# Performance work log

Measured on AMD Instinct MI355X. Metric: run time of the kernel, lower is better.

Reference implementation:

```python
import jax, jax.numpy as jnp
import numpy as np

DIM = 2048
N_HEADS = 16
HEAD_DIM = DIM // N_HEADS
WINDOW = 256
B, S = 2, 2048


def setup_inputs() -> dict:
    key = jax.random.key(0)
    kx, kq, kk, kv, ko = jax.random.split(key, 5)
    bound = 1.0 / np.sqrt(DIM)  # nn.Linear default init range
    x = jax.random.normal(kx, (B, S, DIM), dtype=jnp.float32)
    wq = jax.random.uniform(kq, (DIM, DIM), jnp.float32, -bound, bound)
    wk = jax.random.uniform(kk, (DIM, DIM), jnp.float32, -bound, bound)
    wv = jax.random.uniform(kv, (DIM, DIM), jnp.float32, -bound, bound)
    wo = jax.random.uniform(ko, (DIM, DIM), jnp.float32, -bound, bound)
    return {"x": x, "wq": wq, "wk": wk, "wv": wv, "wo": wo}


def reference(x, wq, wk, wv, wo):
    b, s, d = x.shape
    scale = HEAD_DIM ** -0.5
    # projections (torch Linear: y = x @ W.T)
    q = (x @ wq.T).reshape(b, s, N_HEADS, HEAD_DIM)
    k = (x @ wk.T).reshape(b, s, N_HEADS, HEAD_DIM)
    v = (x @ wv.T).reshape(b, s, N_HEADS, HEAD_DIM)
    # scores: [b, h, i, j]
    scores = jnp.einsum("bihd,bjhd->bhij", q, k) * scale
    # faithful mask: (all-ones, window cleared, then triu(1)) == mask iff j - i > window//2
    idx = jnp.arange(s)
    mask = (idx[None, :] - idx[:, None]) > (WINDOW // 2)  # [s, s] bool, True = masked
    scores = jnp.where(mask[None, None, :, :], -jnp.inf, scores)
    attn = jax.nn.softmax(scores, axis=-1)
    out = jnp.einsum("bhij,bjhd->bihd", attn, v).reshape(b, s, d)
    return out @ wo.T
```

## Files before the change

### kernel.cpp

```cpp
#include <hip/hip_runtime.h>
#include <stdint.h>
#include <stddef.h>

#define DIMN 2048
#define NH 16
#define HD 128
#define SEQ 2048
#define WIN 128

typedef __attribute__((ext_vector_type(4))) float f32x4;
typedef __attribute__((ext_vector_type(8))) short bf16x8;
typedef __attribute__((ext_vector_type(4))) int i32x4;

#define AS1 __attribute__((address_space(1)))
#define AS3 __attribute__((address_space(3)))

__device__ __forceinline__ unsigned short f2bf(float f) {
  union { float f; unsigned u; } v; v.f = f;
  unsigned r = v.u + 0x7FFFu + ((v.u >> 16) & 1u);
  return (unsigned short)(r >> 16);
}

__global__ void cast_bf16_kernel(const float* __restrict__ src,
                                 unsigned short* __restrict__ dst, int n4) {
  int i = blockIdx.x * blockDim.x + threadIdx.x;
  const int stride = gridDim.x * blockDim.x;
  for (; i < n4; i += stride) {
    float4 v = ((const float4*)src)[i];
    ushort4 o;
    o.x = f2bf(v.x); o.y = f2bf(v.y); o.z = f2bf(v.z); o.w = f2bf(v.w);
    ((ushort4*)dst)[i] = o;
  }
}

__global__ void cast4_bf16_kernel(const float* __restrict__ s0, const float* __restrict__ s1,
                                  const float* __restrict__ s2, const float* __restrict__ s3,
                                  unsigned short* __restrict__ dst, int n4) {
  const float* s = (blockIdx.y == 0) ? s0 : (blockIdx.y == 1) ? s1 : (blockIdx.y == 2) ? s2 : s3;
  unsigned short* d = dst + (size_t)blockIdx.y * 4194304;
  int i = blockIdx.x * blockDim.x + threadIdx.x;
  const int stride = gridDim.x * blockDim.x;
  for (; i < n4; i += stride) {
    float4 v = ((const float4*)s)[i];
    ushort4 o;
    o.x = f2bf(v.x); o.y = f2bf(v.y); o.z = f2bf(v.z); o.w = f2bf(v.w);
    ((ushort4*)d)[i] = o;
  }
}

__device__ __forceinline__ void gemm_mainloop_g128(
    const unsigned short* __restrict__ A, const unsigned short* __restrict__ B,
    int m0, int n0, unsigned short* As, unsigned short* Bs, f32x4 acc[4][4]) {
  const int t = threadIdx.x, lane = t & 63, wid = t >> 6;
  const int c = lane & 15, g = lane >> 4;
  const int wr = wid >> 1, wc = wid & 1;

  const int srow = wid * 32 + (lane >> 3);
  const int gslot = (lane & 7) ^ (lane >> 3);
  const unsigned short* ga = A + (size_t)(m0 + srow) * DIMN + gslot * 8;
  const unsigned short* gb = B + (size_t)(n0 + srow) * DIMN + gslot * 8;
  unsigned short* la = As + (size_t)(wid * 32) * 64;
  unsigned short* lb = Bs + (size_t)(wid * 32) * 64;

  const int swc = c & 7;

  for (int k0 = 0; k0 < DIMN; k0 += 64) {
    __syncthreads();
#pragma unroll
    for (int i = 0; i < 4; ++i) {
      __builtin_amdgcn_global_load_lds(
          (const AS1 unsigned*)(ga + (size_t)i * 8 * DIMN + k0),
          (AS3 unsigned*)(la + i * 8 * 64), 16, 0, 0);
      __builtin_amdgcn_global_load_lds(
          (const AS1 unsigned*)(gb + (size_t)i * 8 * DIMN + k0),
          (AS3 unsigned*)(lb + i * 8 * 64), 16, 0, 0);
    }
    __syncthreads();
#pragma unroll
    for (int kk = 0; kk < 2; ++kk) {
      bf16x8 af[4], bfv[4];
#pragma unroll
      for (int mi = 0; mi < 4; ++mi)
        af[mi] = *(const bf16x8*)&As[(wr * 64 + mi * 16 + c) * 64 +
                                     (((kk * 4 + g) ^ swc) * 8)];
#pragma unroll
      for (int ni = 0; ni < 4; ++ni)
        bfv[ni] = *(const bf16x8*)&Bs[(wc * 64 + ni * 16 + c) * 64 +
                                      (((kk * 4 + g) ^ swc) * 8)];
#pragma unroll
      for (int mi = 0; mi < 4; ++mi)
#pragma unroll
        for (int ni = 0; ni < 4; ++ni)
          acc[mi][ni] = __builtin_amdgcn_mfma_f32_16x16x32_bf16(
              af[mi], bfv[ni], acc[mi][ni], 0, 0, 0);
    }
  }
}

__global__ __launch_bounds__(256, 3) void gemm_qkv_kernel(
    const unsigned short* __restrict__ Xb,
    const unsigned short* __restrict__ Wq,
    const unsigned short* __restrict__ Wk,
    const unsigned short* __restrict__ Wv,
    unsigned short* __restrict__ Qb,
    unsigned short* __restrict__ Kb,
    unsigned short* __restrict__ Vt) {
  __shared__ __attribute__((aligned(16))) unsigned short As[128 * 64];
  __shared__ __attribute__((aligned(16))) unsigned short Bs[128 * 64];
  const int z = blockIdx.z;
  const unsigned short* W = (z == 0) ? Wq : (z == 1) ? Wk : Wv;
  const int m0 = blockIdx.y * 128, n0 = blockIdx.x * 128;

  f32x4 acc[4][4];
  const f32x4 zv = {0.f, 0.f, 0.f, 0.f};
#pragma unroll
  for (int i = 0; i < 4; ++i)
#pragma unroll
    for (int j = 0; j < 4; ++j) acc[i][j] = zv;

  gemm_mainloop_g128(Xb, W, m0, n0, As, Bs, acc);

  const int lane = threadIdx.x & 63, wid = threadIdx.x >> 6;
  const int c = lane & 15, g = lane >> 4;
  const int wr = wid >> 1, wc = wid & 1;
  unsigned short* Out01 = (z == 0) ? Qb : Kb;
#pragma unroll
  for (int mi = 0; mi < 4; ++mi) {
#pragma unroll
    for (int ni = 0; ni < 4; ++ni) {
      const int mrow = m0 + wr * 64 + mi * 16 + g * 4;
      const int ncol = n0 + wc * 64 + ni * 16 + c;
      const int h = ncol >> 7, d = ncol & 127;
      const int b = mrow >> 11, s = mrow & 2047;
      if (z < 2) {
#pragma unroll
        for (int j = 0; j < 4; ++j)
          Out01[((size_t)(b * NH + h) * SEQ + s + j) * HD + d] =
              f2bf(acc[mi][ni][j]);
      } else {
        ushort4 pk;
        pk.x = f2bf(acc[mi][ni][0]); pk.y = f2bf(acc[mi][ni][1]);
        pk.z = f2bf(acc[mi][ni][2]); pk.w = f2bf(acc[mi][ni][3]);
        *(ushort4*)&Vt[((size_t)(b * NH + h) * HD + d) * SEQ + s] = pk;
      }
    }
  }
}

__global__ __launch_bounds__(256, 3) void gemm_out_kernel(
    const unsigned short* __restrict__ Ab,
    const unsigned short* __restrict__ Wo,
    float* __restrict__ Cf) {
  __shared__ __attribute__((aligned(16))) unsigned short As[128 * 64];
  __shared__ __attribute__((aligned(16))) unsigned short Bs[128 * 64];
  const int m0 = blockIdx.y * 128, n0 = blockIdx.x * 128;

  f32x4 acc[4][4];
  const f32x4 zv = {0.f, 0.f, 0.f, 0.f};
#pragma unroll
  for (int i = 0; i < 4; ++i)
#pragma unroll
    for (int j = 0; j < 4; ++j) acc[i][j] = zv;

  gemm_mainloop_g128(Ab, Wo, m0, n0, As, Bs, acc);

  const int lane = threadIdx.x & 63, wid = threadIdx.x >> 6;
  const int c = lane & 15, g = lane >> 4;
  const int wr = wid >> 1, wc = wid & 1;
#pragma unroll
  for (int mi = 0; mi < 4; ++mi) {
#pragma unroll
    for (int ni = 0; ni < 4; ++ni) {
      const int mrow = m0 + wr * 64 + mi * 16 + g * 4;
      const int ncol = n0 + wc * 64 + ni * 16 + c;
#pragma unroll
      for (int j = 0; j < 4; ++j)
        Cf[(size_t)(mrow + j) * DIMN + ncol] = acc[mi][ni][j];
    }
  }
}

__global__ __launch_bounds__(256, 2) void attn_kernel(
    const unsigned short* __restrict__ Qg,
    const unsigned short* __restrict__ Kg,
    const unsigned short* __restrict__ Vtg,
    unsigned short* __restrict__ Og) {
  __shared__ __attribute__((aligned(16))) unsigned short Ks[64 * 128];
  __shared__ __attribute__((aligned(16))) unsigned short Vs[128 * 64];
  __shared__ __attribute__((aligned(16))) unsigned short Ps[4 * 32 * 64];

  const int bh = blockIdx.x;
  const int yy = blockIdx.y;
  const int qt = (yy < 8) ? yy : 23 - yy;
  const int q0 = qt * 128;
  const int t = threadIdx.x, wid = t >> 6, lane = t & 63;
  const int c = lane & 15, g = lane >> 4;
  const int swc = c & 7;

  const unsigned short* Kbh = Kg + (size_t)bh * SEQ * HD;
  const unsigned short* Vbh = Vtg + (size_t)bh * HD * SEQ;

  bf16x8 qf[2][4];
#pragma unroll
  for (int mi = 0; mi < 2; ++mi) {
    const unsigned short* qb =
        Qg + ((size_t)bh * SEQ + q0 + wid * 32 + mi * 16 + c) * HD + g * 8;
#pragma unroll
    for (int kk = 0; kk < 4; ++kk) qf[mi][kk] = *(const bf16x8*)(qb + kk * 32);
  }

  f32x4 o[2][8];
  const f32x4 zv = {0.f, 0.f, 0.f, 0.f};
#pragma unroll
  for (int mi = 0; mi < 2; ++mi)
#pragma unroll
    for (int ni = 0; ni < 8; ++ni) o[mi][ni] = zv;
  float M[2][4], L[2][4];
#pragma unroll
  for (int mi = 0; mi < 2; ++mi)
#pragma unroll
    for (int j = 0; j < 4; ++j) { M[mi][j] = -1e30f; L[mi][j] = 0.f; }

  const int ntA = (q0 + 256) >> 6;
  const int nt = (ntA < (SEQ >> 6)) ? ntA : (SEQ >> 6);
  const float kl2e = 0.08838834764831845f * 1.4426950408889634f;

  const int kswz = (t & 15) ^ ((t >> 4) & 7);
  const int vswz = (t & 7) ^ ((t >> 3) & 7);
  const int kgo = (t >> 4) * HD + (t & 15) * 8;
  const int klo = (t >> 4) * 128 + kswz * 8;
  const int vlo = (t >> 3) * 64 + vswz * 8;
  const size_t vgo = (size_t)(t >> 3) * SEQ + (t & 7) * 8;

  i32x4 kc[4], vc[4];
#pragma unroll
  for (int r = 0; r < 4; ++r) {
    kc[r] = *(const i32x4*)(Kbh + (size_t)r * 16 * HD + kgo);
    vc[r] = *(const i32x4*)(Vbh + (size_t)r * 32 * SEQ + vgo);
  }

  for (int tt = 0; tt < nt; ++tt) {
    const int j0 = tt * 64;
    __syncthreads();
#pragma unroll
    for (int r = 0; r < 4; ++r) {
      *(i32x4*)&Ks[r * 2048 + klo] = kc[r];
      *(i32x4*)&Vs[r * 2048 + vlo] = vc[r];
    }
    __syncthreads();
    if (tt + 1 < nt) {
      const int j1 = j0 + 64;
#pragma unroll
      for (int r = 0; r < 4; ++r) {
        kc[r] = *(const i32x4*)(Kbh + (size_t)(j1 + r * 16) * HD + kgo);
        vc[r] = *(const i32x4*)(Vbh + (size_t)r * 32 * SEQ + j1 + vgo);
      }
    }

    f32x4 sc[2][4];
#pragma unroll
    for (int mi = 0; mi < 2; ++mi)
#pragma unroll
      for (int ni = 0; ni < 4; ++ni) sc[mi][ni] = zv;
    __builtin_amdgcn_s_setprio(1);
#pragma unroll
    for (int kk = 0; kk < 4; ++kk) {
#pragma unroll
      for (int ni = 0; ni < 4; ++ni) {
        const bf16x8 kf =
            *(const bf16x8*)&Ks[(ni * 16 + c) * 128 + ((kk * 4 + g) ^ swc) * 8];
        sc[0][ni] = __builtin_amdgcn_mfma_f32_16x16x32_bf16(qf[0][kk], kf, sc[0][ni], 0, 0, 0);
        sc[1][ni] = __builtin_amdgcn_mfma_f32_16x16x32_bf16(qf[1][kk], kf, sc[1][ni], 0, 0, 0);
      }
    }
    __builtin_amdgcn_s_setprio(0);

    if (j0 - q0 >= 128) {
#pragma unroll
      for (int mi = 0; mi < 2; ++mi)
#pragma unroll
        for (int ni = 0; ni < 4; ++ni) {
          const int jg = j0 + ni * 16 + c;
#pragma unroll
          for (int j = 0; j < 4; ++j) {
            const int ig = q0 + wid * 32 + mi * 16 + g * 4 + j;
            if (jg > ig + WIN) sc[mi][ni][j] = -3.0e38f;
          }
        }
    }

    float tmax[2][4], dmax = -3.0e38f;
#pragma unroll
    for (int mi = 0; mi < 2; ++mi)
#pragma unroll
      for (int j = 0; j < 4; ++j) {
        float mx = fmaxf(fmaxf(sc[mi][0][j], sc[mi][1][j]),
                         fmaxf(sc[mi][2][j], sc[mi][3][j]));
        mx = fmaxf(mx, __shfl_xor(mx, 1));
        mx = fmaxf(mx, __shfl_xor(mx, 2));
        mx = fmaxf(mx, __shfl_xor(mx, 4));
        mx = fmaxf(mx, __shfl_xor(mx, 8));
        tmax[mi][j] = mx;
        dmax = fmaxf(dmax, mx - M[mi][j]);
      }
    if (__any(dmax > 64.f)) {
#pragma unroll
      for (int mi = 0; mi < 2; ++mi)
#pragma unroll
        for (int j = 0; j < 4; ++j) {
          const float nm = fmaxf(M[mi][j], tmax[mi][j]);
          const float al = __builtin_amdgcn_exp2f((M[mi][j] - nm) * kl2e);
          M[mi][j] = nm;
          L[mi][j] *= al;
#pragma unroll
          for (int ni = 0; ni < 8; ++ni) o[mi][ni][j] *= al;
        }
    }

    float rs[2][4] = {{0.f, 0.f, 0.f, 0.f}, {0.f, 0.f, 0.f, 0.f}};
#pragma unroll
    for (int mi = 0; mi < 2; ++mi)
#pragma unroll
      for (int ni = 0; ni < 4; ++ni)
#pragma unroll
        for (int j = 0; j < 4; ++j) {
          const float p = __builtin_amdgcn_exp2f((sc[mi][ni][j] - M[mi][j]) * kl2e);
          rs[mi][j] += p;
          const int prow = mi * 16 + g * 4 + j;
          Ps[wid * 2048 + prow * 64 + ((2 * ni + (c >> 3)) ^ (prow & 7)) * 8 + (c & 7)] =
              f2bf(p);
        }
#pragma unroll
    for (int mi = 0; mi < 2; ++mi)
#pragma unroll
      for (int j = 0; j < 4; ++j) {
        float s = rs[mi][j];
        s += __shfl_xor(s, 1);
        s += __shfl_xor(s, 2);
        s += __shfl_xor(s, 4);
        s += __shfl_xor(s, 8);
        L[mi][j] += s;
      }

    __builtin_amdgcn_s_setprio(1);
#pragma unroll
    for (int kk2 = 0; kk2 < 2; ++kk2) {
      bf16x8 pf[2];
#pragma unroll
      for (int mi = 0; mi < 2; ++mi)
        pf[mi] = *(const bf16x8*)&Ps[wid * 2048 + (mi * 16 + c) * 64 +
                                     ((kk2 * 4 + g) ^ swc) * 8];
#pragma unroll
      for (int ni = 0; ni < 8; ++ni) {
        const bf16x8 vf =
            *(const bf16x8*)&Vs[(ni * 16 + c) * 64 + ((kk2 * 4 + g) ^ swc) * 8];
        o[0][ni] = __builtin_amdgcn_mfma_f32_16x16x32_bf16(pf[0], vf, o[0][ni], 0, 0, 0);
        o[1][ni] = __builtin_amdgcn_mfma_f32_16x16x32_bf16(pf[1], vf, o[1][ni], 0, 0, 0);
      }
    }
    __builtin_amdgcn_s_setprio(0);
  }

  const int b = bh >> 4, h = bh & 15;
#pragma unroll
  for (int mi = 0; mi < 2; ++mi)
#pragma unroll
    for (int j = 0; j < 4; ++j) {
      const float inv = 1.0f / L[mi][j];
      const int s = q0 + wid * 32 + mi * 16 + g * 4 + j;
      unsigned short* orow = Og + (size_t)(b * SEQ + s) * DIMN + h * HD;
#pragma unroll
      for (int ni = 0; ni < 8; ++ni) orow[ni * 16 + c] = f2bf(o[mi][ni][j] * inv);
    }
}

extern "C" void kernel_launch(void* const* d_in, const int* in_sizes, int n_in,
                              void* d_out, int out_size, void* d_ws, size_t ws_size,
                              hipStream_t stream) {
  (void)in_sizes; (void)n_in; (void)out_size; (void)ws_size;
  const float* x  = (const float*)d_in[0];
  const float* wq = (const float*)d_in[1];
  const float* wk = (const float*)d_in[2];
  const float* wv = (const float*)d_in[3];
  const float* wo = (const float*)d_in[4];
  float* out = (float*)d_out;

  unsigned short* xb  = (unsigned short*)d_ws;
  unsigned short* wqb = xb  + (size_t)8388608;
  unsigned short* wkb = wqb + (size_t)4194304;
  unsigned short* wvb = wkb + (size_t)4194304;
  unsigned short* wob = wvb + (size_t)4194304;
  unsigned short* Qb  = wob + (size_t)4194304;
  unsigned short* Kb  = Qb  + (size_t)8388608;
  unsigned short* Vt  = Kb  + (size_t)8388608;
  unsigned short* Ab  = Vt  + (size_t)8388608;

  cast_bf16_kernel<<<dim3(1024), dim3(256), 0, stream>>>(x, xb, 2097152);
  cast4_bf16_kernel<<<dim3(512, 4), dim3(256), 0, stream>>>(wq, wk, wv, wo, wqb, 1048576);

  gemm_qkv_kernel<<<dim3(16, 32, 3), dim3(256), 0, stream>>>(xb, wqb, wkb, wvb, Qb, Kb, Vt);
  attn_kernel<<<dim3(32, 16), dim3(256), 0, stream>>>(Qb, Kb, Vt, Ab);
  gemm_out_kernel<<<dim3(16, 32), dim3(256), 0, stream>>>(Ab, wob, out);
}
```

Measured before the change: 376.1 us.

## Double-buffer K/V LDS tiles and defer row-sum shuffle reduction to epilogue

The attention kernel now keeps two LDS buffers for K and V. The next tile is written into the alternate buffer while the current one is used, and the loop needs one barrier per iteration instead of two. The per-tile cross-lane shuffle reduction of the softmax row sums is also moved out of the loop. Each lane keeps a partial sum that is rescaled alongside o and reduced once before the final normalization. LDS use rises by 32KB per block, which may lower occupancy below the launch-bounds target of 2.

```diff
diff --git a/kernel.cpp b/kernel.cpp
--- a/kernel.cpp
+++ b/kernel.cpp
@@ -185,8 +185,8 @@
     const unsigned short* __restrict__ Kg,
     const unsigned short* __restrict__ Vtg,
     unsigned short* __restrict__ Og) {
-  __shared__ __attribute__((aligned(16))) unsigned short Ks[64 * 128];
-  __shared__ __attribute__((aligned(16))) unsigned short Vs[128 * 64];
+  __shared__ __attribute__((aligned(16))) unsigned short Ks[2][64 * 128];
+  __shared__ __attribute__((aligned(16))) unsigned short Vs[2][128 * 64];
   __shared__ __attribute__((aligned(16))) unsigned short Ps[4 * 32 * 64];
 
   const int bh = blockIdx.x;
@@ -238,24 +238,40 @@
     kc[r] = *(const i32x4*)(Kbh + (size_t)r * 16 * HD + kgo);
     vc[r] = *(const i32x4*)(Vbh + (size_t)r * 32 * SEQ + vgo);
   }
-
+#pragma unroll
+  for (int r = 0; r < 4; ++r) {
+    *(i32x4*)&Ks[0][r * 2048 + klo] = kc[r];
+    *(i32x4*)&Vs[0][r * 2048 + vlo] = vc[r];
+  }
+  if (nt > 1) {
+#pragma unroll
+    for (int r = 0; r < 4; ++r) {
+      kc[r] = *(const i32x4*)(Kbh + (size_t)(64 + r * 16) * HD + kgo);
+      vc[r] = *(const i32x4*)(Vbh + (size_t)r * 32 * SEQ + 64 + vgo);
+    }
+  }
+  __syncthreads();
+
+  int cur = 0;
   for (int tt = 0; tt < nt; ++tt) {
     const int j0 = tt * 64;
-    __syncthreads();
-#pragma unroll
-    for (int r = 0; r < 4; ++r) {
-      *(i32x4*)&Ks[r * 2048 + klo] = kc[r];
-      *(i32x4*)&Vs[r * 2048 + vlo] = vc[r];
-    }
-    __syncthreads();
     if (tt + 1 < nt) {
-      const int j1 = j0 + 64;
 #pragma unroll
       for (int r = 0; r < 4; ++r) {
-        kc[r] = *(const i32x4*)(Kbh + (size_t)(j1 + r * 16) * HD + kgo);
-        vc[r] = *(const i32x4*)(Vbh + (size_t)r * 32 * SEQ + j1 + vgo);
-      }
-    }
+        *(i32x4*)&Ks[cur ^ 1][r * 2048 + klo] = kc[r];
+        *(i32x4*)&Vs[cur ^ 1][r * 2048 + vlo] = vc[r];
+      }
+      if (tt + 2 < nt) {
+        const int j2 = j0 + 128;
+#pragma unroll
+        for (int r = 0; r < 4; ++r) {
+          kc[r] = *(const i32x4*)(Kbh + (size_t)(j2 + r * 16) * HD + kgo);
+          vc[r] = *(const i32x4*)(Vbh + (size_t)r * 32 * SEQ + j2 + vgo);
+        }
+      }
+    }
+    const unsigned short* Kc = Ks[cur];
+    const unsigned short* Vc = Vs[cur];
 
     f32x4 sc[2][4];
 #pragma unroll
@@ -268,7 +284,7 @@
 #pragma unroll
       for (int ni = 0; ni < 4; ++ni) {
         const bf16x8 kf =
-            *(const bf16x8*)&Ks[(ni * 16 + c) * 128 + ((kk * 4 + g) ^ swc) * 8];
+            *(const bf16x8*)&Kc[(ni * 16 + c) * 128 + ((kk * 4 + g) ^ swc) * 8];
         sc[0][ni] = __builtin_amdgcn_mfma_f32_16x16x32_bf16(qf[0][kk], kf, sc[0][ni], 0, 0, 0);
         sc[1][ni] = __builtin_amdgcn_mfma_f32_16x16x32_bf16(qf[1][kk], kf, sc[1][ni], 0, 0, 0);
       }
@@ -317,30 +333,22 @@
         }
     }
 
-    float rs[2][4] = {{0.f, 0.f, 0.f, 0.f}, {0.f, 0.f, 0.f, 0.f}};
-#pragma unroll
-    for (int mi = 0; mi < 2; ++mi)
+#pragma unroll
+    for (int mi = 0; mi < 2; ++mi) {
+      float rs0 = 0.f, rs1 = 0.f, rs2 = 0.f, rs3 = 0.f;
 #pragma unroll
       for (int ni = 0; ni < 4; ++ni)
 #pragma unroll
         for (int j = 0; j < 4; ++j) {
           const float p = __builtin_amdgcn_exp2f((sc[mi][ni][j] - M[mi][j]) * kl2e);
-          rs[mi][j] += p;
+          if (j == 0) rs0 += p; else if (j == 1) rs1 += p;
+          else if (j == 2) rs2 += p; else rs3 += p;
           const int prow = mi * 16 + g * 4 + j;
           Ps[wid * 2048 + prow * 64 + ((2 * ni + (c >> 3)) ^ (prow & 7)) * 8 + (c & 7)] =
               f2bf(p);
         }
-#pragma unroll
-    for (int mi = 0; mi < 2; ++mi)
-#pragma unroll
-      for (int j = 0; j < 4; ++j) {
-        float s = rs[mi][j];
-        s += __shfl_xor(s, 1);
-        s += __shfl_xor(s, 2);
-        s += __shfl_xor(s, 4);
-        s += __shfl_xor(s, 8);
-        L[mi][j] += s;
-      }
+      L[mi][0] += rs0; L[mi][1] += rs1; L[mi][2] += rs2; L[mi][3] += rs3;
+    }
 
     __builtin_amdgcn_s_setprio(1);
 #pragma unroll
@@ -353,12 +361,15 @@
 #pragma unroll
       for (int ni = 0; ni < 8; ++ni) {
         const bf16x8 vf =
-            *(const bf16x8*)&Vs[(ni * 16 + c) * 64 + ((kk2 * 4 + g) ^ swc) * 8];
+            *(const bf16x8*)&Vc[(ni * 16 + c) * 64 + ((kk2 * 4 + g) ^ swc) * 8];
         o[0][ni] = __builtin_amdgcn_mfma_f32_16x16x32_bf16(pf[0], vf, o[0][ni], 0, 0, 0);
         o[1][ni] = __builtin_amdgcn_mfma_f32_16x16x32_bf16(pf[1], vf, o[1][ni], 0, 0, 0);
       }
     }
     __builtin_amdgcn_s_setprio(0);
+
+    __syncthreads();
+    cur ^= 1;
   }
 
   const int b = bh >> 4, h = bh & 15;
@@ -366,9 +377,14 @@
   for (int mi = 0; mi < 2; ++mi)
 #pragma unroll
     for (int j = 0; j < 4; ++j) {
-      const float inv = 1.0f / L[mi][j];
-      const int s = q0 + wid * 32 + mi * 16 + g * 4 + j;
-      unsigned short* orow = Og + (size_t)(b * SEQ + s) * DIMN + h * HD;
+      float s = L[mi][j];
+      s += __shfl_xor(s, 1);
+      s += __shfl_xor(s, 2);
+      s += __shfl_xor(s, 4);
+      s += __shfl_xor(s, 8);
+      const float inv = 1.0f / s;
+      const int srow = q0 + wid * 32 + mi * 16 + g * 4 + j;
+      unsigned short* orow = Og + (size_t)(b * SEQ + srow) * DIMN + h * HD;
 #pragma unroll
       for (int ni = 0; ni < 8; ++ni) orow[ni * 16 + c] = f2bf(o[mi][ni][j] * inv);
     }
```

Result: no change. 379.3 us (+0.8%).
